# Optimization experiments

Measured on AMD Instinct MI355X. Metric: run time of the kernel, lower is better.

The kernel has to match this reference:

```python
import jax, jax.numpy as jnp
import numpy as np

FORGET_BIAS = 1.0  # TF BasicLSTMCell default


def setup_inputs() -> dict:
    key = jax.random.key(0)
    k1, k2, k3, k4 = jax.random.split(key, 4)
    B, T, E, H, V = 64, 128, 256, 1024, 32000
    x = jax.random.normal(k1, (B, T, E), dtype=jnp.float32)
    # fused LSTM kernel [(E+H), 4H], gate order i, j, f, o
    kernel = jax.random.normal(k2, (E + H, 4 * H), dtype=jnp.float32) * 0.05
    bias = jnp.zeros((4 * H,), dtype=jnp.float32)
    w_out = jax.random.normal(k3, (H, V), dtype=jnp.float32) * 0.01
    b_out = jax.random.normal(k4, (V,), dtype=jnp.float32)
    return {"x": x, "kernel": kernel, "bias": bias, "w_out": w_out, "b_out": b_out}


def _lstm_last_hidden(x, kernel, bias):
    B, T, E = x.shape
    H = kernel.shape[1] // 4
    c0 = jnp.zeros((B, H), dtype=x.dtype)
    h0 = jnp.zeros((B, H), dtype=x.dtype)

    def step(carry, x_t):
        c, h = carry
        gates = jnp.concatenate([x_t, h], axis=1) @ kernel + bias  # [B, 4H]
        i, j, f, o = jnp.split(gates, 4, axis=1)
        new_c = c * jax.nn.sigmoid(f + FORGET_BIAS) + jax.nn.sigmoid(i) * jnp.tanh(j)
        new_h = jnp.tanh(new_c) * jax.nn.sigmoid(o)
        return (new_c, new_h), None

    (c_T, h_T), _ = jax.lax.scan(step, (c0, h0), jnp.swapaxes(x, 0, 1))
    return h_T  # [B, H]


def reference(x, kernel, bias, w_out, b_out):
    h_last = _lstm_last_hidden(x, kernel, bias)
    return h_last @ w_out + b_out  # [B, V]
```

## Files before the change

kernel.cpp:

```cpp
#include <hip/hip_runtime.h>
#include <hip/hip_bf16.h>
#include <stdint.h>

#define B_ 64
#define T_ 128
#define E_ 256
#define H_ 1024
#define G_ 4096
#define V_ 32000
#define HS_ 65536

typedef __attribute__((ext_vector_type(8))) short short8;
typedef __attribute__((ext_vector_type(4))) float floatx4;
typedef __attribute__((ext_vector_type(4))) unsigned short ushortx4;

static __device__ __forceinline__ unsigned short f2bf(float f){
  union { float f; unsigned u; } v; v.f = f;
  unsigned r = v.u + 0x7FFFu + ((v.u >> 16) & 1u);
  return (unsigned short)(r >> 16);
}
static __device__ __forceinline__ float bf2f(unsigned short s){
  union { unsigned u; float f; } v; v.u = ((unsigned)s) << 16;
  return v.f;
}
static __device__ __forceinline__ float sigmoidf_(float x){
  return 1.0f / (1.0f + __expf(-x));
}
static __device__ __forceinline__ float tanhf_(float x){
  const float a = fabsf(x);
  const float t = 1.0f - 2.0f / (__expf(2.0f * a) + 1.0f);
  return __builtin_copysignf(t, x);
}

__global__ __launch_bounds__(256) void k_transpose(const float* __restrict__ kern,
    unsigned short* __restrict__ wx_t, unsigned short* __restrict__ wh_t){
  __shared__ float tile[32][36];
  const int k0 = blockIdx.x * 32, g0 = blockIdx.y * 32;
  const int r  = threadIdx.x >> 3;
  const int c4 = (threadIdx.x & 7) << 2;
  const float4 v = *reinterpret_cast<const float4*>(kern + (size_t)(k0 + r) * G_ + g0 + c4);
  tile[r][c4 + 0] = v.x; tile[r][c4 + 1] = v.y;
  tile[r][c4 + 2] = v.z; tile[r][c4 + 3] = v.w;
  __syncthreads();
  const unsigned short o0 = f2bf(tile[c4 + 0][r]);
  const unsigned short o1 = f2bf(tile[c4 + 1][r]);
  const unsigned short o2 = f2bf(tile[c4 + 2][r]);
  const unsigned short o3 = f2bf(tile[c4 + 3][r]);
  const ushort4 pk = make_ushort4(o0, o1, o2, o3);
  if (k0 < E_)
    *reinterpret_cast<ushort4*>(wx_t + (size_t)(g0 + r) * E_ + (k0 + c4)) = pk;
  else
    *reinterpret_cast<ushort4*>(wh_t + (size_t)(g0 + r) * H_ + (k0 - E_ + c4)) = pk;
}

__global__ __launch_bounds__(256) void k_xgates(const float* __restrict__ x,
    const unsigned short* __restrict__ wx_t, const float* __restrict__ bias,
    unsigned short* __restrict__ xgp){
  const int w = threadIdx.x >> 6, l = threadIdx.x & 63;
  const int quad = l >> 4, n = l & 15;
  const int Mbase = blockIdx.x * 64 + w * 16;
  const int Nbase = blockIdx.y * 256;
  const int r = Mbase + n;
  const int b = r & 63, t = r >> 6;
  const float* arow = x + ((size_t)b * T_ + t) * E_;
  floatx4 acc[16];
  #pragma unroll
  for (int i = 0; i < 16; ++i) acc[i] = (floatx4){0.f,0.f,0.f,0.f};
  #pragma unroll
  for (int kt = 0; kt < 8; ++kt){
    const int k0 = kt * 32 + quad * 8;
    const float4 f0 = *reinterpret_cast<const float4*>(arow + k0);
    const float4 f1 = *reinterpret_cast<const float4*>(arow + k0 + 4);
    short8 af;
    af[0] = (short)f2bf(f0.x); af[1] = (short)f2bf(f0.y);
    af[2] = (short)f2bf(f0.z); af[3] = (short)f2bf(f0.w);
    af[4] = (short)f2bf(f1.x); af[5] = (short)f2bf(f1.y);
    af[6] = (short)f2bf(f1.z); af[7] = (short)f2bf(f1.w);
    const unsigned short* bp = wx_t + (size_t)(Nbase + n) * E_ + k0;
    #pragma unroll
    for (int nt = 0; nt < 16; ++nt){
      const short8 bf = *reinterpret_cast<const short8*>(bp + (size_t)nt * 16 * E_);
      acc[nt] = __builtin_amdgcn_mfma_f32_16x16x32_bf16(af, bf, acc[nt], 0, 0, 0);
    }
  }
  const int t_out = blockIdx.x;
  const int gate = blockIdx.y >> 2;
  const int np = gate * 4 + (n & 3);
  #pragma unroll
  for (int nt = 0; nt < 16; ++nt){
    const int g = Nbase + nt * 16 + n;
    const float bi = bias[g];
    const int wgd = (blockIdx.y & 3) * 64 + nt * 4 + (n >> 2);
    ushort4 pk;
    pk.x = f2bf(acc[nt][0] + bi);
    pk.y = f2bf(acc[nt][1] + bi);
    pk.z = f2bf(acc[nt][2] + bi);
    pk.w = f2bf(acc[nt][3] + bi);
    *reinterpret_cast<ushort4*>(xgp +
        (((size_t)t_out * 256 + wgd) * 256 + w * 64 + quad * 16 + np) * 4) = pk;
  }
}

__global__ __launch_bounds__(256, 1) void k_lstm(const unsigned short* __restrict__ wh_t,
    const unsigned short* __restrict__ xgp, unsigned short* __restrict__ hb,
    float* __restrict__ hT, unsigned int* __restrict__ bar){
  const int tid = threadIdx.x;
  const int wg = blockIdx.x;
  const int hbase = wg * 4;
  const int w = tid >> 6, l = tid & 63, quad = l >> 4, n = l & 15;
  const int g_lane = (n >> 2) * H_ + hbase + (n & 3);
  const int rowb = w * 16 + quad * 4;
  const bool low8  = (n & 8) == 0;
  const bool first = (n & 4) == 0;

  short8 bfr[32];
  {
    const unsigned short* bp = wh_t + (size_t)g_lane * H_ + quad * 8;
    #pragma unroll
    for (int kt = 0; kt < 32; ++kt)
      bfr[kt] = *reinterpret_cast<const short8*>(bp + kt * 32);
  }
  #pragma unroll
  for (int kt = 0; kt < 32; ++kt)
    __asm__ volatile("" : "+a"(bfr[kt]));

  float creg[4] = {0.f, 0.f, 0.f, 0.f};
  ushortx4 xgv = *reinterpret_cast<const ushortx4*>(xgp + ((size_t)wg * 256 + tid) * 4);

  for (int t = 0; t < T_; ++t){
    const unsigned short* asrc = hb + (size_t)t * HS_ + (size_t)(w * 16 + n) * H_ + quad * 8;
    short8 afr[32];
    #pragma unroll
    for (int kt = 0; kt < 32; ++kt)
      afr[kt] = *reinterpret_cast<const short8*>(asrc + kt * 32);
    #pragma unroll
    for (int kt = 0; kt < 32; ++kt)
      __asm__ volatile("" : "+v"(afr[kt]));

    ushortx4 xgv_n = xgv;
    if (t < T_ - 1){
      xgv_n = *reinterpret_cast<const ushortx4*>(
          xgp + (((size_t)(t + 1) * 256 + wg) * 256 + tid) * 4);
      __asm__ volatile("" : "+v"(xgv_n));
    }

    floatx4 a0 = {0.f,0.f,0.f,0.f}, a1 = {0.f,0.f,0.f,0.f};
    floatx4 a2 = {0.f,0.f,0.f,0.f}, a3 = {0.f,0.f,0.f,0.f};
    #pragma unroll
    for (int kt = 0; kt < 32; kt += 4){
      a0 = __builtin_amdgcn_mfma_f32_16x16x32_bf16(afr[kt + 0], bfr[kt + 0], a0, 0, 0, 0);
      a1 = __builtin_amdgcn_mfma_f32_16x16x32_bf16(afr[kt + 1], bfr[kt + 1], a1, 0, 0, 0);
      a2 = __builtin_amdgcn_mfma_f32_16x16x32_bf16(afr[kt + 2], bfr[kt + 2], a2, 0, 0, 0);
      a3 = __builtin_amdgcn_mfma_f32_16x16x32_bf16(afr[kt + 3], bfr[kt + 3], a3, 0, 0, 0);
    }
    floatx4 acc = (a0 + a1) + (a2 + a3);
    acc[0] += bf2f(xgv[0]); acc[1] += bf2f(xgv[1]);
    acc[2] += bf2f(xgv[2]); acc[3] += bf2f(xgv[3]);

    float r1o[4], q1[4], q2[4];
    #pragma unroll
    for (int reg = 0; reg < 4; ++reg){
      const float a_ = acc[reg];
      const float p_ = __shfl_xor(a_, 4);
      const float x1 = first ? a_ : p_;
      const float x2 = first ? p_ : a_;
      const float s1 = sigmoidf_(low8 ? x1 : (x1 + 1.0f));
      const float r1 = low8 ? s1 * tanhf_(x2) : s1;
      const float r2 = low8 ? 0.0f : sigmoidf_(x2);
      r1o[reg] = r1;
      q1[reg] = __shfl_xor(r1, 8);
      q2[reg] = __shfl_xor(r2, 8);
    }
    if (n < 4){
      unsigned short* hout = hb + (size_t)(t + 1) * HS_;
      #pragma unroll
      for (int reg = 0; reg < 4; ++reg){
        const float cn = creg[reg] * q1[reg] + r1o[reg];
        creg[reg] = cn;
        const float hv = tanhf_(cn) * q2[reg];
        __hip_atomic_store(&hout[(size_t)(rowb + reg) * H_ + hbase + n], f2bf(hv),
                           __ATOMIC_RELAXED, __HIP_MEMORY_SCOPE_AGENT);
        if (t == T_ - 1) hT[(size_t)(hbase + n) * B_ + rowb + reg] = hv;
      }
    }
    if (t < T_ - 1){
      __syncthreads();
      const unsigned step = (unsigned)(t + 1);
      if (tid == 0){
        __asm__ volatile("" ::: "memory");
        __hip_atomic_fetch_add(&bar[(wg & 63) * 32], 1u,
                               __ATOMIC_RELAXED, __HIP_MEMORY_SCOPE_AGENT);
      }
      if (wg == 0){
        if (tid < 64){
          const unsigned tgt = step * 256u;
          for (;;){
            unsigned s = __hip_atomic_load(&bar[tid * 32],
                                           __ATOMIC_RELAXED, __HIP_MEMORY_SCOPE_AGENT);
            s += __shfl_xor(s, 1);  s += __shfl_xor(s, 2);
            s += __shfl_xor(s, 4);  s += __shfl_xor(s, 8);
            s += __shfl_xor(s, 16); s += __shfl_xor(s, 32);
            if (s >= tgt) break;
          }
          if (tid < 16)
            __hip_atomic_store(&bar[2048 + tid * 32], step,
                               __ATOMIC_RELAXED, __HIP_MEMORY_SCOPE_AGENT);
        }
      } else if (tid == 0){
        while (__hip_atomic_load(&bar[2048 + (wg & 15) * 32],
                                 __ATOMIC_RELAXED, __HIP_MEMORY_SCOPE_AGENT) < step) {}
        __asm__ volatile("" ::: "memory");
      }
      __syncthreads();
      xgv = xgv_n;
    }
  }
}

__global__ __launch_bounds__(256) void k_proj(const float* __restrict__ w_out,
    const float* __restrict__ hT, const float* __restrict__ b_out,
    float* __restrict__ out){
  __shared__ float wsh[32 * 68];
  __shared__ float hsh[32 * 68];
  const int tid = threadIdx.x;
  const int vbase = blockIdx.x * 64;
  const int vq = tid & 15, bg = tid >> 4;
  floatx4 acc[4] = {{0,0,0,0},{0,0,0,0},{0,0,0,0},{0,0,0,0}};
  for (int c = 0; c < 32; ++c){
    const int k0 = c * 32;
    __syncthreads();
    #pragma unroll
    for (int i = 0; i < 2; ++i){
      const int flat = tid + i * 256;
      const int row = flat >> 4, c4 = (flat & 15) << 2;
      *reinterpret_cast<float4*>(&wsh[row * 68 + c4]) =
        *reinterpret_cast<const float4*>(w_out + (size_t)(k0 + row) * V_ + vbase + c4);
      *reinterpret_cast<float4*>(&hsh[row * 68 + c4]) =
        *reinterpret_cast<const float4*>(hT + (size_t)(k0 + row) * B_ + c4);
    }
    __syncthreads();
    #pragma unroll 8
    for (int k = 0; k < 32; ++k){
      const floatx4 wv = *reinterpret_cast<const floatx4*>(&wsh[k * 68 + vq * 4]);
      #pragma unroll
      for (int j = 0; j < 4; ++j){
        acc[j] += hsh[k * 68 + bg * 4 + j] * wv;
      }
    }
  }
  const floatx4 bv = *reinterpret_cast<const floatx4*>(b_out + vbase + vq * 4);
  #pragma unroll
  for (int j = 0; j < 4; ++j){
    *reinterpret_cast<floatx4*>(out + (size_t)(bg * 4 + j) * V_ + vbase + vq * 4) = acc[j] + bv;
  }
}

extern "C" void kernel_launch(void* const* d_in, const int* in_sizes, int n_in,
                              void* d_out, int out_size, void* d_ws, size_t ws_size,
                              hipStream_t stream){
  (void)in_sizes; (void)n_in; (void)out_size; (void)ws_size;
  const float* x     = (const float*)d_in[0];
  const float* kern  = (const float*)d_in[1];
  const float* bias  = (const float*)d_in[2];
  const float* w_out = (const float*)d_in[3];
  const float* b_out = (const float*)d_in[4];
  float* out = (float*)d_out;
  char* ws = (char*)d_ws;

  const size_t BAR_OFF = 0;
  const size_t HB_OFF  = 16384;
  const size_t HT_OFF  = HB_OFF + (size_t)129 * 131072;
  const size_t WX_OFF  = HT_OFF + 262144;
  const size_t WH_OFF  = WX_OFF + 2097152;
  const size_t XG_OFF  = WH_OFF + 8388608;

  unsigned int*   bar  = (unsigned int*)(ws + BAR_OFF);
  unsigned short* hb   = (unsigned short*)(ws + HB_OFF);
  float*          hT   = (float*)(ws + HT_OFF);
  unsigned short* wx_t = (unsigned short*)(ws + WX_OFF);
  unsigned short* wh_t = (unsigned short*)(ws + WH_OFF);
  unsigned short* xgp  = (unsigned short*)(ws + XG_OFF);

  hipMemsetAsync(ws, 0, HB_OFF + 131072, stream);
  k_transpose<<<dim3(40, 128), 256, 0, stream>>>(kern, wx_t, wh_t);
  k_xgates<<<dim3(128, 16), 256, 0, stream>>>(x, wx_t, bias, xgp);
  k_lstm<<<dim3(256), 256, 0, stream>>>(wh_t, xgp, hb, hT, bar);
  k_proj<<<dim3(500), 256, 0, stream>>>(w_out, hT, b_out, out);
}
```

Measured before the change: 1.269 ms.

## Replace atomic-add grid barrier with per-block flag stores and min-reduction poll

The grid barrier in the persistent LSTM kernel now has each workgroup store its step number into its own packed flag slot, replacing an atomic fetch-add on 64 padded counters. Workgroup 0 polls all 256 flags with four loads per lane and takes a wave-wide min, then releases the others through broadcast flags. The aim is to cut atomic read-modify-write contention and latency on the per-timestep barrier. The x-gate prefetch for the next step is also dropped in favour of loading the current step's value inside the loop, which may expose that load's latency. The packed flags now share cache lines, so the poller scans fewer lines but the stores contend on them.

```diff
diff --git a/kernel.cpp b/kernel.cpp
--- a/kernel.cpp
+++ b/kernel.cpp
@@ -125,7 +125,6 @@
     __asm__ volatile("" : "+a"(bfr[kt]));
 
   float creg[4] = {0.f, 0.f, 0.f, 0.f};
-  ushortx4 xgv = *reinterpret_cast<const ushortx4*>(xgp + ((size_t)wg * 256 + tid) * 4);
 
   for (int t = 0; t < T_; ++t){
     const unsigned short* asrc = hb + (size_t)t * HS_ + (size_t)(w * 16 + n) * H_ + quad * 8;
@@ -133,16 +132,11 @@
     #pragma unroll
     for (int kt = 0; kt < 32; ++kt)
       afr[kt] = *reinterpret_cast<const short8*>(asrc + kt * 32);
+    const ushortx4 xgv = *reinterpret_cast<const ushortx4*>(
+        xgp + (((size_t)t * 256 + wg) * 256 + tid) * 4);
     #pragma unroll
     for (int kt = 0; kt < 32; ++kt)
       __asm__ volatile("" : "+v"(afr[kt]));
-
-    ushortx4 xgv_n = xgv;
-    if (t < T_ - 1){
-      xgv_n = *reinterpret_cast<const ushortx4*>(
-          xgp + (((size_t)(t + 1) * 256 + wg) * 256 + tid) * 4);
-      __asm__ volatile("" : "+v"(xgv_n));
-    }
 
     floatx4 a0 = {0.f,0.f,0.f,0.f}, a1 = {0.f,0.f,0.f,0.f};
     floatx4 a2 = {0.f,0.f,0.f,0.f}, a3 = {0.f,0.f,0.f,0.f};
@@ -188,31 +182,39 @@
       const unsigned step = (unsigned)(t + 1);
       if (tid == 0){
         __asm__ volatile("" ::: "memory");
-        __hip_atomic_fetch_add(&bar[(wg & 63) * 32], 1u,
-                               __ATOMIC_RELAXED, __HIP_MEMORY_SCOPE_AGENT);
+        __hip_atomic_store(&bar[wg], step,
+                           __ATOMIC_RELAXED, __HIP_MEMORY_SCOPE_AGENT);
       }
       if (wg == 0){
         if (tid < 64){
-          const unsigned tgt = step * 256u;
           for (;;){
-            unsigned s = __hip_atomic_load(&bar[tid * 32],
-                                           __ATOMIC_RELAXED, __HIP_MEMORY_SCOPE_AGENT);
-            s += __shfl_xor(s, 1);  s += __shfl_xor(s, 2);
-            s += __shfl_xor(s, 4);  s += __shfl_xor(s, 8);
-            s += __shfl_xor(s, 16); s += __shfl_xor(s, 32);
-            if (s >= tgt) break;
+            const unsigned f0 = __hip_atomic_load(&bar[tid * 4 + 0],
+                                  __ATOMIC_RELAXED, __HIP_MEMORY_SCOPE_AGENT);
+            const unsigned f1 = __hip_atomic_load(&bar[tid * 4 + 1],
+                                  __ATOMIC_RELAXED, __HIP_MEMORY_SCOPE_AGENT);
+            const unsigned f2 = __hip_atomic_load(&bar[tid * 4 + 2],
+                                  __ATOMIC_RELAXED, __HIP_MEMORY_SCOPE_AGENT);
+            const unsigned f3 = __hip_atomic_load(&bar[tid * 4 + 3],
+                                  __ATOMIC_RELAXED, __HIP_MEMORY_SCOPE_AGENT);
+            unsigned m = min(min(f0, f1), min(f2, f3));
+            m = min(m, (unsigned)__shfl_xor((int)m, 1));
+            m = min(m, (unsigned)__shfl_xor((int)m, 2));
+            m = min(m, (unsigned)__shfl_xor((int)m, 4));
+            m = min(m, (unsigned)__shfl_xor((int)m, 8));
+            m = min(m, (unsigned)__shfl_xor((int)m, 16));
+            m = min(m, (unsigned)__shfl_xor((int)m, 32));
+            if (m >= step) break;
           }
           if (tid < 16)
-            __hip_atomic_store(&bar[2048 + tid * 32], step,
+            __hip_atomic_store(&bar[512 + tid * 32], step,
                                __ATOMIC_RELAXED, __HIP_MEMORY_SCOPE_AGENT);
         }
       } else if (tid == 0){
-        while (__hip_atomic_load(&bar[2048 + (wg & 15) * 32],
+        while (__hip_atomic_load(&bar[512 + (wg & 15) * 32],
                                  __ATOMIC_RELAXED, __HIP_MEMORY_SCOPE_AGENT) < step) {}
         __asm__ volatile("" ::: "memory");
       }
       __syncthreads();
-      xgv = xgv_n;
     }
   }
 }
@@ -268,7 +270,7 @@
   char* ws = (char*)d_ws;
 
   const size_t BAR_OFF = 0;
-  const size_t HB_OFF  = 16384;
+  const size_t HB_OFF  = 4096;
   const size_t HT_OFF  = HB_OFF + (size_t)129 * 131072;
   const size_t WX_OFF  = HT_OFF + 262144;
   const size_t WH_OFF  = WX_OFF + 2097152;
```

Result: no change. 1.248 ms (-1.6%).
